# Kernel tuning notes

Measured on AMD Instinct MI355X. Metric: run time of the kernel, lower is better.

Reference implementation:

```python
import jax, jax.numpy as jnp
import numpy as np

HEAD_NUM = 16

def setup_inputs() -> dict:
    key = jax.random.key(0)
    ks = jax.random.split(key, 5)
    B, N, D = 2, 2048, 1024
    x = jax.random.normal(ks[0], (B, N, D), dtype=jnp.float32)
    scale = 0.02
    W_q = jax.random.normal(ks[1], (D, D), dtype=jnp.float32) * scale
    W_k = jax.random.normal(ks[2], (D, D), dtype=jnp.float32) * scale
    W_v = jax.random.normal(ks[3], (D, D), dtype=jnp.float32) * scale
    W_o = jax.random.normal(ks[4], (D, D), dtype=jnp.float32) * scale
    return {"x": x, "W_q": W_q, "W_k": W_k, "W_v": W_v, "W_o": W_o}

def reference(x, W_q, W_k, W_v, W_o):
    B, N, D = x.shape
    H = HEAD_NUM
    hd = D // H  # head_dim
    inv_sqrt_hd = 1.0 / np.sqrt(hd).astype(np.float32)

    def split_head(t):
        # einops 'b n (d h) -> b h n d' : head index is the INNER factor
        return t.reshape(B, N, hd, H).transpose(0, 3, 1, 2)  # [B,H,N,hd]

    # nn.Linear(bias=False): y = x @ W.T
    Q = split_head(x @ W_q.T)
    K = split_head(x @ W_k.T)
    V = split_head(x @ W_v.T)

    scores = jnp.einsum('bhnd,bhmd->bhnm', Q, K) * inv_sqrt_hd  # [B,H,N,N]
    attn = jax.nn.softmax(scores, axis=-1)
    heads = jnp.einsum('bhnm,bhmd->bhnd', attn, V)  # [B,H,N,hd]

    # einops 'b h n d -> b n (h d)' : head index is the OUTER factor here
    concat = heads.transpose(0, 2, 1, 3).reshape(B, N, D)
    return concat @ W_o.T
```

## Files before the change

kernel.cpp:

```cpp
#include <hip/hip_runtime.h>
#include <hip/hip_bf16.h>

typedef __bf16 bf16_t;
typedef __attribute__((ext_vector_type(8))) __bf16 bf16x8;
typedef __attribute__((ext_vector_type(4))) __bf16 bf16x4;
typedef __attribute__((ext_vector_type(4))) float f32x4;
typedef __attribute__((ext_vector_type(16))) float f32x16;

#define MFMA16(A,B,C) __builtin_amdgcn_mfma_f32_16x16x32_bf16((A),(B),(C),0,0,0)
#define MFMA32(A,B,C) __builtin_amdgcn_mfma_f32_32x32x16_bf16((A),(B),(C),0,0,0)

#define BATCH 2
#define SEQ 2048
#define DMODEL 1024
#define NHEAD 16
#define HDIM 64
#define MROWS (BATCH * SEQ)

__device__ __forceinline__ void async16(const bf16_t* g, bf16_t* l) {
    __builtin_amdgcn_global_load_lds(
        (const __attribute__((address_space(1))) unsigned int*)g,
        (__attribute__((address_space(3))) unsigned int*)l, 16, 0, 0);
}

__device__ __forceinline__ bf16x8 ldsA32(const bf16_t* base, int row, int chunk) {
    return *(const bf16x8*)&base[row * 32 + ((chunk ^ ((row >> 1) & 3)) << 3)];
}

__device__ __forceinline__ unsigned pk(float a, float b) {
    union { unsigned u; bf16_t h[2]; } t;
    t.h[0] = (bf16_t)a;
    t.h[1] = (bf16_t)b;
    return t.u;
}

__device__ __forceinline__ void plane32_swap(unsigned& d, unsigned& s) {
    asm("v_permlane32_swap_b32 %0, %1" : "+v"(d), "+v"(s));
}

__device__ __forceinline__ void sm_pack(const f32x16& st, float* rsp, bf16x8* pf) {
    float pexp[16];
#pragma unroll
    for (int r = 0; r < 16; ++r)
        pexp[r] = __builtin_amdgcn_exp2f(st[r]);
    rsp[0] += pexp[0] + pexp[4] + pexp[8] + pexp[12];
    rsp[1] += pexp[1] + pexp[5] + pexp[9] + pexp[13];
    rsp[2] += pexp[2] + pexp[6] + pexp[10] + pexp[14];
    rsp[3] += pexp[3] + pexp[7] + pexp[11] + pexp[15];
#pragma unroll
    for (int s1 = 0; s1 < 2; ++s1) {
        unsigned lo01 = pk(pexp[8 * s1 + 0], pexp[8 * s1 + 1]);
        unsigned lo23 = pk(pexp[8 * s1 + 2], pexp[8 * s1 + 3]);
        unsigned hi01 = pk(pexp[8 * s1 + 4], pexp[8 * s1 + 5]);
        unsigned hi23 = pk(pexp[8 * s1 + 6], pexp[8 * s1 + 7]);
        plane32_swap(lo01, hi01);
        plane32_swap(lo23, hi23);
        union { bf16x8 v; unsigned u[4]; } outv;
        outv.u[0] = lo01;
        outv.u[1] = lo23;
        outv.u[2] = hi01;
        outv.u[3] = hi23;
        pf[s1] = outv.v;
    }
}

__global__ void split_kernel(const float* __restrict__ x, const float* __restrict__ Wq,
                             const float* __restrict__ Wk, const float* __restrict__ Wv,
                             const float* __restrict__ Wo, bf16_t* __restrict__ xh,
                             bf16_t* __restrict__ wh) {
    int blk = blockIdx.x;
    if (blk < 4096) {
        int i = blk * 256 + threadIdx.x;
        f32x4 v = ((const f32x4*)x)[i];
        bf16x4 h;
#pragma unroll
        for (int c = 0; c < 4; ++c) h[c] = (bf16_t)v[c];
        ((bf16x4*)xh)[i] = h;
        return;
    }
    int e = blk - 4096;
    int z = e >> 10;
    int i = (e & 1023) * 256 + threadIdx.x;
    const float* src = (z == 0) ? Wq : (z == 1) ? Wk : (z == 2) ? Wv : Wo;
    const float scale = (z == 0) ? 0.125f * 1.44269504088896f : 1.0f;
    int row = i >> 8, col4 = i & 255;
    int r_src;
    if (z < 3) {
        int h = row >> 6, d = row & 63;
        r_src = 16 * d + h;
    } else {
        r_src = row;
    }
    f32x4 v = ((const f32x4*)src)[r_src * 256 + col4];
    bf16x4 h4;
#pragma unroll
    for (int c = 0; c < 4; ++c) h4[c] = (bf16_t)(v[c] * scale);
    ((bf16x4*)(wh + (size_t)z * DMODEL * DMODEL))[i] = h4;
}

__global__ __launch_bounds__(256)
void gemm_qkv_kernel(const bf16_t* __restrict__ Ah, const bf16_t* __restrict__ Bh0,
                     bf16_t* __restrict__ Coh0, bf16_t* __restrict__ Vt,
                     int M, int Nn, int Kk) {
    __shared__ __align__(16) bf16_t smem[2][8192];

    const int id = blockIdx.x;
    const int xcd = id & 7;
    const int t = id >> 3;
    const int n0i = t & 7;
    const int u = t >> 3;
    const int z = u >> 2;
    const int m0g = u & 3;
    const int m0 = (m0g * 8 + xcd) * 128;
    const int n0 = n0i * 128;

    const bf16_t* Bh = Bh0 + (size_t)z * Nn * Kk;
    const int tid = threadIdx.x;
    const int wave = tid >> 6, lane = tid & 63, lq = lane >> 4, ln = lane & 15;
    const int wr = wave >> 1, wc = wave & 1;

    const bf16_t* g_ptr[4];
    int l_off[4];
#pragma unroll
    for (int q = 0; q < 4; ++q) {
        int e = wave * 4 + q;
        int a = e >> 3, uu = e & 7;
        int C = uu * 64 + lane;
        int r = C >> 2, p = C & 3;
        int c = p ^ ((r >> 1) & 3);
        g_ptr[q] = (a == 0 ? Ah + (size_t)(m0 + r) * Kk
                           : Bh + (size_t)(n0 + r) * Kk) + c * 8;
        l_off[q] = a * 4096 + uu * 512;
    }

    f32x4 acc[4][4] = {};

#pragma unroll
    for (int q = 0; q < 4; ++q)
        async16(g_ptr[q], &smem[0][l_off[q]]);

    const int NIT = Kk / 32;
    for (int j = 0; j < NIT; ++j) {
        __syncthreads();
        if (j + 1 < NIT) {
#pragma unroll
            for (int q = 0; q < 4; ++q)
                async16(g_ptr[q] + (j + 1) * 32, &smem[(j + 1) & 1][l_off[q]]);
        }
        const bf16_t* cur = smem[j & 1];

        bf16x8 ah[4], bh[4];
#pragma unroll
        for (int tt = 0; tt < 4; ++tt) {
            ah[tt] = ldsA32(cur, wr * 64 + tt * 16 + ln, lq);
            bh[tt] = ldsA32(cur + 4096, wc * 64 + tt * 16 + ln, lq);
        }
#pragma unroll
        for (int tm = 0; tm < 4; ++tm)
#pragma unroll
            for (int tn = 0; tn < 4; ++tn)
                acc[tm][tn] = MFMA16(ah[tm], bh[tn], acc[tm][tn]);
    }

    if (z != 2) {
#pragma unroll
        for (int tm = 0; tm < 4; ++tm)
#pragma unroll
            for (int tn = 0; tn < 4; ++tn)
#pragma unroll
                for (int p = 0; p < 4; ++p) {
                    int gm = m0 + wr * 64 + tm * 16 + lq * 4 + p;
                    int gn = n0 + wc * 64 + tn * 16 + ln;
                    Coh0[(size_t)z * M * Nn + (size_t)gm * Nn + gn] =
                        (bf16_t)acc[tm][tn][p];
                }
    } else {
#pragma unroll
        for (int tm = 0; tm < 4; ++tm)
#pragma unroll
            for (int tn = 0; tn < 4; ++tn) {
                int gn = n0 + wc * 64 + tn * 16 + ln;
                int hh = gn >> 6, dd = gn & 63;
                int gm0 = m0 + wr * 64 + tm * 16 + lq * 4;
                int bb = gm0 >> 11, nn = gm0 & 2047;
                bf16x4 v4;
#pragma unroll
                for (int p = 0; p < 4; ++p) v4[p] = (bf16_t)acc[tm][tn][p];
                *(bf16x4*)&Vt[(((size_t)(bb * NHEAD + hh)) * HDIM + dd) * SEQ + nn] = v4;
            }
    }
}

__global__ __launch_bounds__(256)
void gemm_out_kernel(const bf16_t* __restrict__ Ah, const bf16_t* __restrict__ Bh,
                     float* __restrict__ Cf, int M, int Nn, int Kk) {
    __shared__ __align__(16) bf16_t smem[2][6144];

    const int id = blockIdx.x;
    const int xcd = id & 7;
    const int t = id >> 3;
    const int n0i = t & 7;
    const int m0g = t >> 3;
    const int m0 = (m0g * 8 + xcd) * 64;
    const int n0 = n0i * 128;

    const int tid = threadIdx.x;
    const int wave = tid >> 6, lane = tid & 63, lq = lane >> 4, ln = lane & 15;
    const int wr = wave >> 1, wc = wave & 1;

    const bf16_t* g_ptr[3];
    int l_off[3];
#pragma unroll
    for (int q = 0; q < 3; ++q) {
        int e = wave * 3 + q;
        const bf16_t* arr;
        int u, rowbase, lb;
        if (e < 4) { arr = Ah; u = e;     rowbase = m0; lb = 0; }
        else       { arr = Bh; u = e - 4; rowbase = n0; lb = 2048; }
        int r = u * 16 + (lane >> 2), p = lane & 3;
        int c = p ^ ((r >> 1) & 3);
        g_ptr[q] = arr + (size_t)(rowbase + r) * Kk + c * 8;
        l_off[q] = lb + u * 512;
    }

    f32x4 acc[2][4] = {};

#pragma unroll
    for (int q = 0; q < 3; ++q)
        async16(g_ptr[q], &smem[0][l_off[q]]);

    const int NIT = Kk / 32;
    for (int j = 0; j < NIT; ++j) {
        __syncthreads();
        if (j + 1 < NIT) {
#pragma unroll
            for (int q = 0; q < 3; ++q)
                async16(g_ptr[q] + (j + 1) * 32, &smem[(j + 1) & 1][l_off[q]]);
        }
        const bf16_t* cur = smem[j & 1];

        bf16x8 ah[2], bh[4];
#pragma unroll
        for (int tt = 0; tt < 2; ++tt)
            ah[tt] = ldsA32(cur, wr * 32 + tt * 16 + ln, lq);
#pragma unroll
        for (int tt = 0; tt < 4; ++tt)
            bh[tt] = ldsA32(cur + 2048, wc * 64 + tt * 16 + ln, lq);
#pragma unroll
        for (int tm = 0; tm < 2; ++tm)
#pragma unroll
            for (int tn = 0; tn < 4; ++tn)
                acc[tm][tn] = MFMA16(ah[tm], bh[tn], acc[tm][tn]);
    }

#pragma unroll
    for (int tm = 0; tm < 2; ++tm)
#pragma unroll
        for (int tn = 0; tn < 4; ++tn)
#pragma unroll
            for (int p = 0; p < 4; ++p) {
                int gm = m0 + wr * 32 + tm * 16 + lq * 4 + p;
                int gn = n0 + wc * 64 + tn * 16 + ln;
                Cf[(size_t)gm * Nn + gn] = acc[tm][tn][p];
            }
}

__global__ __launch_bounds__(256, 2)
void attn_kernel(const bf16_t* __restrict__ Qh, const bf16_t* __restrict__ Kh,
                 const bf16_t* __restrict__ Vt, bf16_t* __restrict__ Ch) {
    __shared__ __align__(16) bf16_t smem[2][4][4096];

    const int id = blockIdx.x;
    const int bh = ((id >> 7) << 3) | (id & 7);
    const int qt = (id >> 3) & 15;
    const int b = bh >> 4, h = bh & 15;
    const int q0 = qt * 128;
    const int tid = threadIdx.x;
    const int g = tid >> 7;
    const int wv = (tid >> 6) & 1;
    const int lane = tid & 63;
    const int ln32 = lane & 31, hl = lane >> 5;

    bf16x8 qfh[2][4];
#pragma unroll
    for (int qs = 0; qs < 2; ++qs) {
        size_t qrow = ((size_t)(b * SEQ + q0 + wv * 64 + qs * 32 + ln32)) * DMODEL +
                      h * HDIM + hl * 8;
#pragma unroll
        for (int c = 0; c < 4; ++c)
            qfh[qs][c] = *(const bf16x8*)&Qh[qrow + c * 16];
    }
    asm volatile("s_waitcnt vmcnt(0)" ::: "memory");

    int xcK[4];
#pragma unroll
    for (int c = 0; c < 4; ++c)
        xcK[c] = (((2 * c + hl) ^ (ln32 & 7)) << 3) + ln32 * 64;
    int xcV[2];
#pragma unroll
    for (int s = 0; s < 2; ++s)
        xcV[s] = (((2 * s + hl) ^ ((ln32 >> 1) & 3)) << 3) + ln32 * 32;

    bf16_t* gsm = &smem[g][0][0];
    const bf16_t* gb;
    size_t ustep, jstep;
    int lb;
    if (wv == 0) {
        int r0 = lane >> 3, p = lane & 7;
        int c = p ^ (r0 & 7);
        gb = Kh + ((size_t)(b * SEQ + g * 1024 + r0)) * DMODEL + h * HDIM + c * 8;
        ustep = (size_t)8 * DMODEL;
        jstep = (size_t)32 * DMODEL;
        lb = 0;
    } else {
        int r0 = lane >> 2, p = lane & 3;
        int c = p ^ ((r0 >> 1) & 3);
        gb = Vt + ((size_t)(bh * HDIM + r0)) * SEQ + g * 1024 + c * 8;
        ustep = (size_t)16 * SEQ;
        jstep = 32;
        lb = 2048;
    }

    f32x16 o[2][2];
#pragma unroll
    for (int qs = 0; qs < 2; ++qs)
#pragma unroll
        for (int dt = 0; dt < 2; ++dt)
#pragma unroll
            for (int r = 0; r < 16; ++r) o[qs][dt][r] = 0.0f;
    float rsA[4] = {0.f, 0.f, 0.f, 0.f};
    float rsB[4] = {0.f, 0.f, 0.f, 0.f};

#pragma unroll
    for (int tix = 0; tix < 3; ++tix)
#pragma unroll
        for (int u = 0; u < 4; ++u)
            async16(gb + (size_t)tix * jstep + u * ustep,
                    gsm + tix * 4096 + lb + u * 512);

    for (int j = 0; j < 32; ++j) {
        asm volatile("s_waitcnt vmcnt(8)" ::: "memory");
        __builtin_amdgcn_s_barrier();
        __builtin_amdgcn_sched_barrier(0);
        {
            int idx = (j + 3 < 32) ? (j + 3) : 31;
            const bf16_t* gsrc = gb + (size_t)idx * jstep;
            bf16_t* ldst = gsm + (idx & 3) * 4096 + lb;
#pragma unroll
            for (int u = 0; u < 4; ++u)
                async16(gsrc + u * ustep, ldst + u * 512);
        }
        const bf16_t* Kc = gsm + (j & 3) * 4096;
        const bf16_t* Vc = Kc + 2048;

        bf16x8 kh[4];
#pragma unroll
        for (int c = 0; c < 4; ++c)
            kh[c] = *(const bf16x8*)&Kc[xcK[c]];
        f32x16 s0, s1;
#pragma unroll
        for (int r = 0; r < 16; ++r) { s0[r] = 0.0f; s1[r] = 0.0f; }
        __builtin_amdgcn_s_setprio(1);
#pragma unroll
        for (int c = 0; c < 4; ++c)
            s0 = MFMA32(kh[c], qfh[0][c], s0);
#pragma unroll
        for (int c = 0; c < 4; ++c)
            s1 = MFMA32(kh[c], qfh[1][c], s1);
        __builtin_amdgcn_s_setprio(0);
        bf16x8 pfA[2], pfB[2];
        sm_pack(s0, rsA, pfA);
        sm_pack(s1, rsB, pfB);
        __builtin_amdgcn_s_setprio(1);
#pragma unroll
        for (int s = 0; s < 2; ++s) {
            bf16x8 va0 = *(const bf16x8*)&Vc[xcV[s]];
            bf16x8 va1 = *(const bf16x8*)&Vc[1024 + xcV[s]];
            o[0][0] = MFMA32(va0, pfA[s], o[0][0]);
            o[0][1] = MFMA32(va1, pfA[s], o[0][1]);
            o[1][0] = MFMA32(va0, pfB[s], o[1][0]);
            o[1][1] = MFMA32(va1, pfB[s], o[1][1]);
        }
        __builtin_amdgcn_s_setprio(0);
    }

    float rs[2];
    rs[0] = (rsA[0] + rsA[1]) + (rsA[2] + rsA[3]);
    rs[1] = (rsB[0] + rsB[1]) + (rsB[2] + rsB[3]);
#pragma unroll
    for (int qs = 0; qs < 2; ++qs)
        rs[qs] += __shfl_xor(rs[qs], 32);

    __syncthreads();
    float* cbuf = (float*)smem;
    float* rbuf = cbuf + 8192;
    if (g == 1) {
#pragma unroll
        for (int qs = 0; qs < 2; ++qs)
#pragma unroll
            for (int dt = 0; dt < 2; ++dt)
#pragma unroll
                for (int r = 0; r < 16; ++r) {
                    int d = dt * 32 + (r & 3) + 8 * (r >> 2) + 4 * hl;
                    cbuf[d * 128 + wv * 64 + qs * 32 + ln32] = o[qs][dt][r];
                }
        if (hl == 0) {
            rbuf[wv * 64 + ln32] = rs[0];
            rbuf[wv * 64 + 32 + ln32] = rs[1];
        }
    }
    __syncthreads();
    float inv[2] = {0.0f, 0.0f};
    if (g == 0) {
#pragma unroll
        for (int qs = 0; qs < 2; ++qs) {
#pragma unroll
            for (int dt = 0; dt < 2; ++dt)
#pragma unroll
                for (int r = 0; r < 16; ++r) {
                    int d = dt * 32 + (r & 3) + 8 * (r >> 2) + 4 * hl;
                    o[qs][dt][r] += cbuf[d * 128 + wv * 64 + qs * 32 + ln32];
                }
            inv[qs] = 1.0f / (rs[qs] + rbuf[wv * 64 + qs * 32 + ln32]);
        }
    }
    __syncthreads();
    float* fbuf = (float*)smem;
    if (g == 0) {
#pragma unroll
        for (int qs = 0; qs < 2; ++qs)
#pragma unroll
            for (int dh = 0; dh < 2; ++dh)
#pragma unroll
                for (int r = 0; r < 16; ++r) {
                    int d_loc = (r & 3) + 8 * (r >> 2) + 4 * hl;
                    fbuf[dh * 4224 + (wv * 2 + qs) * 1056 + ln32 * 33 + d_loc] =
                        o[qs][dh][r] * inv[qs];
                }
    }
    __syncthreads();
    {
        int gw = tid >> 6;
        int dh = gw >> 1, wpair = gw & 1;
#pragma unroll
        for (int ww = 0; ww < 2; ++ww) {
            int w = wpair * 2 + ww;
#pragma unroll
            for (int qq = 0; qq < 16; ++qq) {
                int qrow = hl * 16 + qq;
                float v = fbuf[dh * 4224 + w * 1056 + qrow * 33 + ln32];
                size_t gidx = ((size_t)(b * SEQ + q0 + w * 32 + qrow)) * DMODEL +
                              h * HDIM + dh * 32 + ln32;
                Ch[gidx] = (bf16_t)v;
            }
        }
    }
}

extern "C" void kernel_launch(void* const* d_in, const int* in_sizes, int n_in,
                              void* d_out, int out_size, void* d_ws, size_t ws_size,
                              hipStream_t stream) {
    const float* x  = (const float*)d_in[0];
    const float* Wq = (const float*)d_in[1];
    const float* Wk = (const float*)d_in[2];
    const float* Wv = (const float*)d_in[3];
    const float* Wo = (const float*)d_in[4];
    float* out = (float*)d_out;

    char* ws = (char*)d_ws;
    size_t off = 0;
    auto alloc = [&](size_t bytes) -> bf16_t* {
        bf16_t* p = (bf16_t*)(ws + off);
        off += (bytes + 255) & ~(size_t)255;
        return p;
    };
    const size_t XE = (size_t)MROWS * DMODEL;
    const size_t WE = (size_t)DMODEL * DMODEL;

    bf16_t* xh  = alloc(XE * 2);
    bf16_t* wh  = alloc(4 * WE * 2);
    bf16_t* qnh = alloc(3 * XE * 2);
    bf16_t* vth = alloc(XE * 2);
    bf16_t* ch  = alloc(XE * 2);
    (void)ws_size; (void)in_sizes; (void)n_in; (void)out_size;

    split_kernel<<<8192, 256, 0, stream>>>(x, Wq, Wk, Wv, Wo, xh, wh);

    gemm_qkv_kernel<<<768, 256, 0, stream>>>(xh, wh, qnh, vth, MROWS, DMODEL, DMODEL);

    attn_kernel<<<512, 256, 0, stream>>>(qnh, qnh + XE, vth, ch);

    gemm_out_kernel<<<512, 256, 0, stream>>>(ch, wh + 3 * WE, out, MROWS, DMODEL, DMODEL);
}
```

Before: 177.5 us.

## Split attention KV range across four wave groups with 512-thread blocks

Each attention block now has 512 threads organised as four groups, and each group handles 512 keys instead of 1024, doubling the waves available per query tile. The 4-deep async prefetch ring with explicit vmcnt waits is replaced by a per-group double buffer synchronised with __syncthreads. The aim is more latency hiding and MFMA occupancy. In exchange, the partial-output reduction grows to three serial LDS rounds, and there are more block-wide barriers per tile. Score accumulators now start from a zero vector fed into the first MFMA rather than being cleared each iteration.

```diff
diff --git a/kernel.cpp b/kernel.cpp
--- a/kernel.cpp
+++ b/kernel.cpp
@@ -265,10 +265,10 @@
             }
 }
 
-__global__ __launch_bounds__(256, 2)
+__global__ __launch_bounds__(512, 4)
 void attn_kernel(const bf16_t* __restrict__ Qh, const bf16_t* __restrict__ Kh,
                  const bf16_t* __restrict__ Vt, bf16_t* __restrict__ Ch) {
-    __shared__ __align__(16) bf16_t smem[2][4][4096];
+    __shared__ __align__(16) bf16_t smem[4][2][4096];
 
     const int id = blockIdx.x;
     const int bh = ((id >> 7) << 3) | (id & 7);
@@ -290,7 +290,6 @@
         for (int c = 0; c < 4; ++c)
             qfh[qs][c] = *(const bf16x8*)&Qh[qrow + c * 16];
     }
-    asm volatile("s_waitcnt vmcnt(0)" ::: "memory");
 
     int xcK[4];
 #pragma unroll
@@ -308,14 +307,14 @@
     if (wv == 0) {
         int r0 = lane >> 3, p = lane & 7;
         int c = p ^ (r0 & 7);
-        gb = Kh + ((size_t)(b * SEQ + g * 1024 + r0)) * DMODEL + h * HDIM + c * 8;
+        gb = Kh + ((size_t)(b * SEQ + g * 512 + r0)) * DMODEL + h * HDIM + c * 8;
         ustep = (size_t)8 * DMODEL;
         jstep = (size_t)32 * DMODEL;
         lb = 0;
     } else {
         int r0 = lane >> 2, p = lane & 3;
         int c = p ^ ((r0 >> 1) & 3);
-        gb = Vt + ((size_t)(bh * HDIM + r0)) * SEQ + g * 1024 + c * 8;
+        gb = Vt + ((size_t)(bh * HDIM + r0)) * SEQ + g * 512 + c * 8;
         ustep = (size_t)16 * SEQ;
         jstep = 32;
         lb = 2048;
@@ -328,44 +327,40 @@
         for (int dt = 0; dt < 2; ++dt)
 #pragma unroll
             for (int r = 0; r < 16; ++r) o[qs][dt][r] = 0.0f;
+    f32x16 zacc;
+#pragma unroll
+    for (int r = 0; r < 16; ++r) zacc[r] = 0.0f;
     float rsA[4] = {0.f, 0.f, 0.f, 0.f};
     float rsB[4] = {0.f, 0.f, 0.f, 0.f};
 
 #pragma unroll
-    for (int tix = 0; tix < 3; ++tix)
-#pragma unroll
-        for (int u = 0; u < 4; ++u)
-            async16(gb + (size_t)tix * jstep + u * ustep,
-                    gsm + tix * 4096 + lb + u * 512);
-
-    for (int j = 0; j < 32; ++j) {
-        asm volatile("s_waitcnt vmcnt(8)" ::: "memory");
-        __builtin_amdgcn_s_barrier();
-        __builtin_amdgcn_sched_barrier(0);
-        {
-            int idx = (j + 3 < 32) ? (j + 3) : 31;
-            const bf16_t* gsrc = gb + (size_t)idx * jstep;
-            bf16_t* ldst = gsm + (idx & 3) * 4096 + lb;
+    for (int u = 0; u < 4; ++u)
+        async16(gb + u * ustep, gsm + lb + u * 512);
+    gb += jstep;
+
+    for (int j = 0; j < 16; ++j) {
+        __syncthreads();
+        if (j < 15) {
 #pragma unroll
             for (int u = 0; u < 4; ++u)
-                async16(gsrc + u * ustep, ldst + u * 512);
-        }
-        const bf16_t* Kc = gsm + (j & 3) * 4096;
+                async16(gb + u * ustep, gsm + ((j + 1) & 1) * 4096 + lb + u * 512);
+            gb += jstep;
+        }
+        const bf16_t* Kc = gsm + (j & 1) * 4096;
         const bf16_t* Vc = Kc + 2048;
 
         bf16x8 kh[4];
 #pragma unroll
         for (int c = 0; c < 4; ++c)
             kh[c] = *(const bf16x8*)&Kc[xcK[c]];
-        f32x16 s0, s1;
-#pragma unroll
-        for (int r = 0; r < 16; ++r) { s0[r] = 0.0f; s1[r] = 0.0f; }
         __builtin_amdgcn_s_setprio(1);
-#pragma unroll
-        for (int c = 0; c < 4; ++c)
+        f32x16 s0 = MFMA32(kh[0], qfh[0][0], zacc);
+        f32x16 s1 = MFMA32(kh[0], qfh[1][0], zacc);
+#pragma unroll
+        for (int c = 1; c < 4; ++c)
             s0 = MFMA32(kh[c], qfh[0][c], s0);
 #pragma unroll
-        for (int c = 0; c < 4; ++c)
+        for (int c = 1; c < 4; ++c)
             s1 = MFMA32(kh[c], qfh[1][c], s1);
         __builtin_amdgcn_s_setprio(0);
         bf16x8 pfA[2], pfB[2];
@@ -394,37 +389,42 @@
     __syncthreads();
     float* cbuf = (float*)smem;
     float* rbuf = cbuf + 8192;
-    if (g == 1) {
-#pragma unroll
-        for (int qs = 0; qs < 2; ++qs)
-#pragma unroll
-            for (int dt = 0; dt < 2; ++dt)
-#pragma unroll
-                for (int r = 0; r < 16; ++r) {
-                    int d = dt * 32 + (r & 3) + 8 * (r >> 2) + 4 * hl;
-                    cbuf[d * 128 + wv * 64 + qs * 32 + ln32] = o[qs][dt][r];
-                }
-        if (hl == 0) {
-            rbuf[wv * 64 + ln32] = rs[0];
-            rbuf[wv * 64 + 32 + ln32] = rs[1];
-        }
-    }
-    __syncthreads();
-    float inv[2] = {0.0f, 0.0f};
-    if (g == 0) {
-#pragma unroll
-        for (int qs = 0; qs < 2; ++qs) {
-#pragma unroll
-            for (int dt = 0; dt < 2; ++dt)
-#pragma unroll
-                for (int r = 0; r < 16; ++r) {
-                    int d = dt * 32 + (r & 3) + 8 * (r >> 2) + 4 * hl;
-                    o[qs][dt][r] += cbuf[d * 128 + wv * 64 + qs * 32 + ln32];
-                }
-            inv[qs] = 1.0f / (rs[qs] + rbuf[wv * 64 + qs * 32 + ln32]);
-        }
-    }
-    __syncthreads();
+    for (int gg = 1; gg < 4; ++gg) {
+        if (g == gg) {
+#pragma unroll
+            for (int qs = 0; qs < 2; ++qs)
+#pragma unroll
+                for (int dt = 0; dt < 2; ++dt)
+#pragma unroll
+                    for (int r = 0; r < 16; ++r) {
+                        int d = dt * 32 + (r & 3) + 8 * (r >> 2) + 4 * hl;
+                        cbuf[d * 128 + wv * 64 + qs * 32 + ln32] = o[qs][dt][r];
+                    }
+            if (hl == 0) {
+                rbuf[wv * 64 + ln32] = rs[0];
+                rbuf[wv * 64 + 32 + ln32] = rs[1];
+            }
+        }
+        __syncthreads();
+        if (g == 0) {
+#pragma unroll
+            for (int qs = 0; qs < 2; ++qs) {
+#pragma unroll
+                for (int dt = 0; dt < 2; ++dt)
+#pragma unroll
+                    for (int r = 0; r < 16; ++r) {
+                        int d = dt * 32 + (r & 3) + 8 * (r >> 2) + 4 * hl;
+                        o[qs][dt][r] += cbuf[d * 128 + wv * 64 + qs * 32 + ln32];
+                    }
+                rs[qs] += rbuf[wv * 64 + qs * 32 + ln32];
+            }
+        }
+        __syncthreads();
+    }
+    float inv[2];
+    inv[0] = (g == 0) ? 1.0f / rs[0] : 0.0f;
+    inv[1] = (g == 0) ? 1.0f / rs[1] : 0.0f;
+
     float* fbuf = (float*)smem;
     if (g == 0) {
 #pragma unroll
@@ -441,18 +441,14 @@
     __syncthreads();
     {
         int gw = tid >> 6;
-        int dh = gw >> 1, wpair = gw & 1;
-#pragma unroll
-        for (int ww = 0; ww < 2; ++ww) {
-            int w = wpair * 2 + ww;
-#pragma unroll
-            for (int qq = 0; qq < 16; ++qq) {
-                int qrow = hl * 16 + qq;
-                float v = fbuf[dh * 4224 + w * 1056 + qrow * 33 + ln32];
-                size_t gidx = ((size_t)(b * SEQ + q0 + w * 32 + qrow)) * DMODEL +
-                              h * HDIM + dh * 32 + ln32;
-                Ch[gidx] = (bf16_t)v;
-            }
+        int dh = gw >> 2, w = gw & 3;
+#pragma unroll
+        for (int qq = 0; qq < 16; ++qq) {
+            int qrow = hl * 16 + qq;
+            float v = fbuf[dh * 4224 + w * 1056 + qrow * 33 + ln32];
+            size_t gidx = ((size_t)(b * SEQ + q0 + w * 32 + qrow)) * DMODEL +
+                          h * HDIM + dh * 32 + ln32;
+            Ch[gidx] = (bf16_t)v;
         }
     }
 }
@@ -488,7 +484,7 @@
 
     gemm_qkv_kernel<<<768, 256, 0, stream>>>(xh, wh, qnh, vth, MROWS, DMODEL, DMODEL);
 
-    attn_kernel<<<512, 256, 0, stream>>>(qnh, qnh + XE, vth, ch);
+    attn_kernel<<<512, 512, 0, stream>>>(qnh, qnh + XE, vth, ch);
 
     gemm_out_kernel<<<512, 256, 0, stream>>>(ch, wh + 3 * WE, out, MROWS, DMODEL, DMODEL);
 }
```

New measurement: 381.3 us. 115% more time.
